# Kernel optimization log

Measured on AMD Instinct MI355X. Metric: run time of the kernel, lower is better.

The kernel has to match this reference:

```python
import jax, jax.numpy as jnp
import numpy as np
import math

E = 2048        # embed_dim
H = 16          # num_heads
HD = E // H // 2  # head_dim = 64
DEPTH = 12
LAMBDA_INIT = 0.8 - 0.6 * math.exp(-0.3 * DEPTH)


def setup_inputs() -> dict:
    key = jax.random.key(0)
    ks = jax.random.split(key, 9)
    s = 0.02
    return {
        "x": jax.random.normal(ks[0], (2, 2048, E), jnp.float32),
        "Wq": jax.random.normal(ks[1], (E, E), jnp.float32) * s,
        "Wk": jax.random.normal(ks[2], (E, E), jnp.float32) * s,  # n_rep = 1
        "Wv": jax.random.normal(ks[3], (E, E), jnp.float32) * s,
        "Wo": jax.random.normal(ks[4], (E, E), jnp.float32) * s,
        "lq1": jax.random.normal(ks[5], (HD,), jnp.float32) * 0.1,
        "lk1": jax.random.normal(ks[6], (HD,), jnp.float32) * 0.1,
        "lq2": jax.random.normal(ks[7], (HD,), jnp.float32) * 0.1,
        "lk2": jax.random.normal(ks[8], (HD,), jnp.float32) * 0.1,
    }


def reference(x, Wq, Wk, Wv, Wo, lq1, lk1, lq2, lk2):
    b, t, e = x.shape
    scaling = HD ** (-0.5)
    # projections; split into 2*H sub-heads of dim HD for q/k, H heads of 2*HD for v
    q = (x @ Wq).reshape(b, t, 2 * H, HD).transpose(0, 2, 1, 3) * scaling  # [b,2H,t,hd]
    k = (x @ Wk).reshape(b, t, 2 * H, HD).transpose(0, 2, 1, 3)           # [b,2H,t,hd]
    v = (x @ Wv).reshape(b, t, H, 2 * HD).transpose(0, 2, 1, 3)           # [b,H,t,2hd]

    scores = jnp.einsum('bhqd,bhkd->bhqk', q, k)  # [b,2H,t,t]
    causal = jnp.triu(jnp.full((t, t), -jnp.inf, dtype=jnp.float32), 1)
    aw = jax.nn.softmax((scores + causal).astype(jnp.float32), axis=-1)

    lam = (jnp.exp(jnp.sum(lq1 * lk1)) - jnp.exp(jnp.sum(lq2 * lk2)) + LAMBDA_INIT)
    aw = aw.reshape(b, H, 2, t, t)
    aw = aw[:, :, 0] - lam * aw[:, :, 1]  # differential attention

    attn = jnp.einsum('bhqk,bhkd->bhqd', aw, v)  # [b,H,t,2hd]
    # RMSNorm over last dim (no affine), eps=1e-5
    attn = attn * jax.lax.rsqrt(jnp.mean(attn * attn, axis=-1, keepdims=True) + 1e-5)
    attn = attn * (1.0 - LAMBDA_INIT)
    attn = attn.transpose(0, 2, 1, 3).reshape(b, t, H * 2 * HD)
    return attn @ Wo
```

## Files before the change

### kernel.cpp

```cpp
#include <hip/hip_runtime.h>
#include <stdint.h>

typedef __bf16 bf16_t;
typedef __bf16 bf16x8 __attribute__((ext_vector_type(8)));
typedef __bf16 bf16x4 __attribute__((ext_vector_type(4)));
typedef float  f32x4  __attribute__((ext_vector_type(4)));
typedef float  f32x16 __attribute__((ext_vector_type(16)));
typedef unsigned int u32;

#define L2E 1.44269504088896340736f
#define LAMBDA_INIT 0.7836057665316245f
#define ONE_MINUS_LAMBDA_INIT 0.2163942334683755f

__device__ __forceinline__ void gload_lds16(const void* g, void* l) {
  __builtin_amdgcn_global_load_lds(
      (const __attribute__((address_space(1))) char*)(uintptr_t)g,
      (__attribute__((address_space(3))) char*)(uintptr_t)l, 16, 0, 0);
}

__device__ __forceinline__ f32x4 mfma_bf16(bf16x8 a, bf16x8 b, f32x4 c) {
  return __builtin_amdgcn_mfma_f32_16x16x32_bf16(a, b, c, 0, 0, 0);
}
__device__ __forceinline__ f32x16 mfma32(bf16x8 a, bf16x8 b, f32x16 c) {
  return __builtin_amdgcn_mfma_f32_32x32x16_bf16(a, b, c, 0, 0, 0);
}

__device__ __forceinline__ u32 pkbf(float a, float b) {
  union { bf16_t h[2]; u32 u; } x;
  x.h[0] = (bf16_t)a; x.h[1] = (bf16_t)b;
  return x.u;
}
__device__ __forceinline__ void pl32swap(u32& a, u32& b) {
  asm volatile("v_permlane32_swap_b32 %0, %1" : "+v"(a), "+v"(b));
}

__global__ __launch_bounds__(256) void cvt_bf16(const float* __restrict__ in,
                                                bf16_t* __restrict__ out) {
  const size_t idx = ((size_t)blockIdx.x * 256 + threadIdx.x) * 8;
  float4 a = *(const float4*)(in + idx);
  float4 c = *(const float4*)(in + idx + 4);
  bf16x8 v;
  v[0] = (bf16_t)a.x; v[1] = (bf16_t)a.y; v[2] = (bf16_t)a.z; v[3] = (bf16_t)a.w;
  v[4] = (bf16_t)c.x; v[5] = (bf16_t)c.y; v[6] = (bf16_t)c.z; v[7] = (bf16_t)c.w;
  *(bf16x8*)(out + idx) = v;
}

struct WArgs {
  const float* W[4];
  bf16_t* WT[4];
  float sc[4];
};

__global__ __launch_bounds__(256) void cvt_wT_all(WArgs a) {
  __shared__ float t[64][65];
  const int i = blockIdx.z;
  const float* W = a.W[i];
  bf16_t* WT = a.WT[i];
  const float scale = a.sc[i];
  const int k0 = blockIdx.x * 64, n0 = blockIdx.y * 64;
  const int r = threadIdx.x >> 2, cg = threadIdx.x & 3;
#pragma unroll
  for (int q = 0; q < 4; ++q) {
    float4 v = *(const float4*)(W + (size_t)(k0 + r) * 2048 + n0 + cg * 16 + q * 4);
    t[r][cg * 16 + q * 4 + 0] = v.x;
    t[r][cg * 16 + q * 4 + 1] = v.y;
    t[r][cg * 16 + q * 4 + 2] = v.z;
    t[r][cg * 16 + q * 4 + 3] = v.w;
  }
  __syncthreads();
  bf16x8 o0, o1;
#pragma unroll
  for (int j = 0; j < 8; ++j) o0[j] = (bf16_t)(t[cg * 16 + j][r] * scale);
#pragma unroll
  for (int j = 0; j < 8; ++j) o1[j] = (bf16_t)(t[cg * 16 + 8 + j][r] * scale);
  bf16_t* dst = WT + (size_t)(n0 + r) * 2048 + k0 + cg * 16;
  *(bf16x8*)dst = o0;
  *(bf16x8*)(dst + 8) = o1;
}

__global__ void lam_kernel(const float* lq1, const float* lk1,
                           const float* lq2, const float* lk2, float* out) {
  const int l = threadIdx.x;
  float p1 = lq1[l] * lk1[l];
  float p2 = lq2[l] * lk2[l];
#pragma unroll
  for (int d = 1; d < 64; d <<= 1) {
    p1 += __shfl_xor(p1, d);
    p2 += __shfl_xor(p2, d);
  }
  if (l == 0) *out = expf(p1) - expf(p2) + LAMBDA_INIT;
}

__global__ __launch_bounds__(512, 2) void gemm256(const bf16_t* __restrict__ A,
                                                  const bf16_t* __restrict__ Bt,
                                                  bf16_t* __restrict__ Cqk) {
  extern __shared__ __align__(16) char sm[];
  const int tid = threadIdx.x;
  const int w = tid >> 6, lane = tid & 63;
  const int wr = w >> 2, wc = w & 3;
  const int lm = lane >> 4, ln = lane & 15;
  const int nwg = (int)(gridDim.x * gridDim.y);
  const int flat = (int)blockIdx.y * (int)gridDim.x + (int)blockIdx.x;
  const int swz = (flat & 7) * (nwg >> 3) + (flat >> 3);
  const int m0 = (swz & 15) * 256, n0 = (swz >> 4) * 256;

  int aoff[8], boff[4];
#pragma unroll
  for (int m = 0; m < 8; ++m) {
    const int row = wr * 128 + m * 16 + ln;
    aoff[m] = row * 64 + ((lm * 16) ^ ((((row >> 2) ^ row) & 3) << 4));
  }
#pragma unroll
  for (int n = 0; n < 4; ++n) {
    const int row = wc * 64 + n * 16 + ln;
    boff[n] = row * 64 + ((lm * 16) ^ ((((row >> 2) ^ row) & 3) << 4));
  }

  const bf16_t* gsrc[4];
  int ldst[4];
#pragma unroll
  for (int j = 0; j < 4; ++j) {
    const int r2 = j & 1, opB = j >> 1;
    const int row = r2 * 128 + w * 16 + (lane >> 2);
    const int colb = (lane & 3) * 16;
    const int cb = colb ^ ((((row >> 2) ^ row) & 3) << 4);
    gsrc[j] = (opB ? Bt + (size_t)(n0 + row) * 2048
                   : A + (size_t)(m0 + row) * 2048) + (cb >> 1);
    ldst[j] = opB * 16384 + r2 * 8192 + w * 1024;
  }

  const f32x4 vzero = {0.f, 0.f, 0.f, 0.f};
  f32x4 acc[8][4];
#pragma unroll
  for (int m = 0; m < 8; ++m)
#pragma unroll
    for (int n = 0; n < 4; ++n) acc[m][n] = vzero;

#pragma unroll
  for (int kt = 0; kt < 3; ++kt)
#pragma unroll
    for (int j = 0; j < 4; ++j)
      gload_lds16(gsrc[j] + kt * 32, sm + kt * 32768 + ldst[j]);
  asm volatile("s_waitcnt vmcnt(8)" ::: "memory");
  __builtin_amdgcn_s_barrier();

  for (int kt = 0; kt < 64; ++kt) {
    const char* sa = sm + (kt & 3) * 32768;
    const char* sb = sa + 16384;
    const int stage = kt + 3;
    char* sd = sm + (stage & 3) * 32768;
    bf16x8 bfr[4], af[4];

#pragma unroll
    for (int n = 0; n < 4; ++n) bfr[n] = *(const bf16x8*)(sb + boff[n]);
#pragma unroll
    for (int m = 0; m < 4; ++m) af[m] = *(const bf16x8*)(sa + aoff[m]);
    if (stage < 64) {
      gload_lds16(gsrc[0] + stage * 32, sd + ldst[0]);
      gload_lds16(gsrc[1] + stage * 32, sd + ldst[1]);
    }
    __builtin_amdgcn_s_barrier();
    __builtin_amdgcn_s_setprio(1);
#pragma unroll
    for (int m = 0; m < 4; ++m)
#pragma unroll
      for (int n = 0; n < 4; ++n) acc[m][n] = mfma_bf16(af[m], bfr[n], acc[m][n]);
    __builtin_amdgcn_s_setprio(0);
    __builtin_amdgcn_s_barrier();

#pragma unroll
    for (int m = 0; m < 4; ++m) af[m] = *(const bf16x8*)(sa + aoff[4 + m]);
    if (stage < 64) {
      gload_lds16(gsrc[2] + stage * 32, sd + ldst[2]);
      gload_lds16(gsrc[3] + stage * 32, sd + ldst[3]);
    }
    __builtin_amdgcn_s_barrier();
    __builtin_amdgcn_s_setprio(1);
#pragma unroll
    for (int m = 0; m < 4; ++m)
#pragma unroll
      for (int n = 0; n < 4; ++n)
        acc[4 + m][n] = mfma_bf16(af[m], bfr[n], acc[4 + m][n]);
    __builtin_amdgcn_s_setprio(0);
    if (kt < 61) {
      asm volatile("s_waitcnt vmcnt(8)" ::: "memory");
    } else if (kt == 61) {
      asm volatile("s_waitcnt vmcnt(4)" ::: "memory");
    } else if (kt == 62) {
      asm volatile("s_waitcnt vmcnt(0)" ::: "memory");
    }
    __builtin_amdgcn_s_barrier();
  }

  bf16_t* C = Cqk + (size_t)(n0 >> 11) * (4096u * 2048u);
#pragma unroll
  for (int m = 0; m < 8; ++m)
#pragma unroll
    for (int n = 0; n < 4; ++n)
#pragma unroll
      for (int r = 0; r < 4; ++r) {
        const size_t grow = m0 + wr * 128 + m * 16 + lm * 4 + r;
        const int gcol = (n0 + wc * 64 + n * 16 + ln) & 2047;
        C[grow * 2048 + gcol] = (bf16_t)acc[m][n][r];
      }
}

template <int OUTMODE>
__global__ __launch_bounds__(256, 2) void gemm_bt(const bf16_t* __restrict__ A,
                                                  const bf16_t* __restrict__ Bt,
                                                  void* __restrict__ Cv) {
  __shared__ __align__(16) bf16_t As[128 * 64];
  __shared__ __align__(16) bf16_t Bs[128 * 64];
  const int tid = threadIdx.x;
  const int w = tid >> 6, lane = tid & 63;
  const int wr = w >> 1, wc = w & 1;
  const int lm = lane >> 4, ln = lane & 15;
  const int nwg = (int)(gridDim.x * gridDim.y);
  const int flat = (int)blockIdx.y * (int)gridDim.x + (int)blockIdx.x;
  const int swz = (flat & 7) * (nwg >> 3) + (flat >> 3);
  const int m0 = (swz & 31) * 128, n0 = (swz >> 5) * 128;

  const f32x4 vzero = {0.f, 0.f, 0.f, 0.f};
  f32x4 acc[4][4];
#pragma unroll
  for (int m = 0; m < 4; ++m)
#pragma unroll
    for (int n = 0; n < 4; ++n) acc[m][n] = vzero;

  for (int k0 = 0; k0 < 2048; k0 += 64) {
    __syncthreads();
#pragma unroll
    for (int j = 0; j < 4; ++j) {
      const int inst = w * 4 + j;
      const int row = inst * 8 + (lane >> 3);
      const int cb = ((lane & 7) * 16) ^ ((row & 7) << 4);
      gload_lds16(A + (size_t)(m0 + row) * 2048 + k0 + (cb >> 1),
                  (char*)As + inst * 1024);
      gload_lds16(Bt + (size_t)(n0 + row) * 2048 + k0 + (cb >> 1),
                  (char*)Bs + inst * 1024);
    }
    asm volatile("s_waitcnt vmcnt(0)" ::: "memory");
    __syncthreads();

#pragma unroll
    for (int kc = 0; kc < 2; ++kc) {
      bf16x8 af[4], bfr[4];
#pragma unroll
      for (int m = 0; m < 4; ++m) {
        const int row = wr * 64 + m * 16 + ln;
        int off = row * 128 + kc * 64 + lm * 16;
        off ^= (row & 7) << 4;
        af[m] = *(const bf16x8*)((const char*)As + off);
      }
#pragma unroll
      for (int n = 0; n < 4; ++n) {
        const int row = wc * 64 + n * 16 + ln;
        int off = row * 128 + kc * 64 + lm * 16;
        off ^= (row & 7) << 4;
        bfr[n] = *(const bf16x8*)((const char*)Bs + off);
      }
      __builtin_amdgcn_s_setprio(1);
#pragma unroll
      for (int m = 0; m < 4; ++m)
#pragma unroll
        for (int n = 0; n < 4; ++n) acc[m][n] = mfma_bf16(af[m], bfr[n], acc[m][n]);
      __builtin_amdgcn_s_setprio(0);
    }
  }

  if (OUTMODE == 1) {
    bf16_t* C = (bf16_t*)Cv;
#pragma unroll
    for (int m = 0; m < 4; ++m) {
      const int growb = m0 + wr * 64 + m * 16 + lm * 4;
      const int bb = growb >> 11, t = growb & 2047;
      const int kt = t >> 6, kk = (t >> 4) & 3, hi2 = (t >> 3) & 1, e0 = t & 7;
#pragma unroll
      for (int n = 0; n < 4; ++n) {
        const int gcol = n0 + wc * 64 + n * 16 + ln;
        const int hh = gcol >> 7, g = (gcol >> 5) & 3, l31o = gcol & 31;
        bf16x4 v;
#pragma unroll
        for (int r = 0; r < 4; ++r) v[r] = (bf16_t)acc[m][n][r];
        const size_t idx = ((size_t)((bb * 16 + hh) * 32 + kt)) * 8192 +
                           (size_t)(((g * 4 + kk) * 64 + hi2 * 32 + l31o) * 8 + e0);
        *(bf16x4*)(C + idx) = v;
      }
    }
  } else {
    float* C = (float*)Cv;
#pragma unroll
    for (int m = 0; m < 4; ++m)
#pragma unroll
      for (int n = 0; n < 4; ++n)
#pragma unroll
        for (int r = 0; r < 4; ++r) {
          const size_t grow = m0 + wr * 64 + m * 16 + lm * 4 + r;
          const int gcol = n0 + wc * 64 + n * 16 + ln;
          C[grow * 2048 + gcol] = acc[m][n][r];
        }
  }
}

__global__ __launch_bounds__(256, 2) void flash_diff(const bf16_t* __restrict__ Q,
                                                     const bf16_t* __restrict__ K,
                                                     const bf16_t* __restrict__ Vf,
                                                     bf16_t* __restrict__ attnb,
                                                     const float* __restrict__ lamP) {
  __shared__ __align__(16) char smem[65536];

  const int tid = threadIdx.x;
  const int w = tid >> 6, lane = tid & 63;
  const int qh = w >> 1, s = w & 1;
  const int l31 = lane & 31, hi = lane >> 5;

  const int bid = (int)blockIdx.x;
  const int xcd = bid & 7, p = bid >> 3;
  const int qtp = p & 15, g2 = p >> 4;
  const int hb = g2 * 8 + xcd;
  const int h = hb & 15, b = hb >> 4;
  const size_t bt0 = (size_t)b * 2048;
  const float lam = *lamP;

  auto stage_k = [&](int buf, int k0) {
#pragma unroll
    for (int j = 0; j < 4; ++j) {
      const int inst = w * 4 + j;
      const int row = inst * 4 + (lane >> 4);
      const int cb = ((lane & 15) * 16) ^ ((row & 15) << 4);
      gload_lds16(K + (bt0 + k0 + row) * 2048 + h * 128 + (cb >> 1),
                  smem + buf * 16384 + inst * 1024);
    }
  };
  auto stage_v = [&](int buf, int kt) {
    const char* src = (const char*)Vf +
                      (((size_t)((b * 16 + h) * 32 + kt)) << 14) + lane * 16;
#pragma unroll
    for (int j = 0; j < 4; ++j) {
      const int inst = w * 4 + j;
      gload_lds16(src + inst * 1024, smem + 32768 + buf * 16384 + inst * 1024);
    }
  };

  for (int half = 0; half < 2; ++half) {
    const int qt = half == 0 ? qtp : 31 - qtp;
    const int q0 = qt * 64;
    const int qloc = qh * 32 + l31;

    bf16x8 qf[4];
#pragma unroll
    for (int kc = 0; kc < 4; ++kc)
      qf[kc] = *(const bf16x8*)(Q + (bt0 + q0 + qloc) * 2048 + h * 128 +
                                s * 64 + kc * 16 + hi * 8);

    stage_k(0, 0);
    stage_v(0, 0);
    asm volatile("s_waitcnt vmcnt(0)" ::: "memory");
    __syncthreads();

    f32x16 accv[4];
#pragma unroll
    for (int m = 0; m < 4; ++m)
#pragma unroll
      for (int r = 0; r < 16; ++r) accv[m][r] = 0.f;
    float lsum = 0.f;

    int cur = 0;
    for (int kt = 0; kt <= qt; ++kt) {
      if (kt < qt) {
        stage_k(cur ^ 1, (kt + 1) * 64);
        stage_v(cur ^ 1, kt + 1);
      }
      const char* Ksb = (const char*)smem + cur * 16384;
      const char* Vsb = (const char*)smem + 32768 + cur * 16384;

      bf16x8 pf[2][2];
#pragma unroll
      for (int mt = 0; mt < 2; ++mt) {
        f32x16 sa;
#pragma unroll
        for (int r = 0; r < 16; ++r) sa[r] = 0.f;
        const int row = mt * 32 + l31;
        const int rswz = (row & 15) << 4;
        __builtin_amdgcn_s_setprio(1);
#pragma unroll
        for (int kc = 0; kc < 4; ++kc) {
          int off = row * 256 + s * 128 + kc * 32 + hi * 16;
          off ^= rswz;
          bf16x8 kf = *(const bf16x8*)(Ksb + off);
          sa = mfma32(kf, qf[kc], sa);
        }
        __builtin_amdgcn_s_setprio(0);

        if (kt == qt) {
#pragma unroll
          for (int r = 0; r < 16; ++r) {
            const int key = mt * 32 + (r & 3) + 8 * (r >> 2) + 4 * hi;
            if (key > qloc) sa[r] = -1e30f;
          }
        }
        float pv[16];
#pragma unroll
        for (int r = 0; r < 16; ++r) {
          pv[r] = exp2f(sa[r]);
          lsum += pv[r];
        }
        u32 c0 = pkbf(pv[0], pv[1]),   c1 = pkbf(pv[2], pv[3]);
        u32 c2 = pkbf(pv[4], pv[5]),   c3 = pkbf(pv[6], pv[7]);
        u32 c4 = pkbf(pv[8], pv[9]),   c5 = pkbf(pv[10], pv[11]);
        u32 c6 = pkbf(pv[12], pv[13]), c7 = pkbf(pv[14], pv[15]);
        pl32swap(c0, c2); pl32swap(c1, c3);
        pl32swap(c4, c6); pl32swap(c5, c7);
        union { u32 u[4]; bf16x8 v; } f0, f1;
        f0.u[0] = c0; f0.u[1] = c1; f0.u[2] = c2; f0.u[3] = c3;
        f1.u[0] = c4; f1.u[1] = c5; f1.u[2] = c6; f1.u[3] = c7;
        pf[mt][0] = f0.v;
        pf[mt][1] = f1.v;
      }

#pragma unroll
      for (int g = 0; g < 4; ++g) {
        __builtin_amdgcn_s_setprio(1);
#pragma unroll
        for (int kk = 0; kk < 4; ++kk) {
          bf16x8 vfr = *(const bf16x8*)(Vsb + (g * 4 + kk) * 1024 + lane * 16);
          accv[g] = mfma32(vfr, pf[kk >> 1][kk & 1], accv[g]);
        }
        __builtin_amdgcn_s_setprio(0);
      }

      asm volatile("s_waitcnt vmcnt(0)" ::: "memory");
      __syncthreads();
      cur ^= 1;
    }

    lsum += __shfl_xor(lsum, 32);
    const float rl = 1.0f / lsum;
    float* Obuf = (float*)smem;

    if (s == 1) {
#pragma unroll
      for (int mt4 = 0; mt4 < 4; ++mt4)
#pragma unroll
        for (int q2 = 0; q2 < 4; ++q2) {
          f32x4 v;
#pragma unroll
          for (int e = 0; e < 4; ++e) v[e] = accv[mt4][q2 * 4 + e] * rl;
          const int d = mt4 * 32 + q2 * 8 + hi * 4;
          *(f32x4*)(Obuf + (size_t)qloc * 128 + d) = v;
        }
    }
    __syncthreads();
    if (s == 0) {
      float o[4][16];
      float ss = 0.f;
#pragma unroll
      for (int mt4 = 0; mt4 < 4; ++mt4)
#pragma unroll
        for (int q2 = 0; q2 < 4; ++q2) {
          const int d = mt4 * 32 + q2 * 8 + hi * 4;
          f32x4 ov = *(const f32x4*)(Obuf + (size_t)qloc * 128 + d);
#pragma unroll
          for (int e = 0; e < 4; ++e) {
            const float v = accv[mt4][q2 * 4 + e] * rl - lam * ov[e];
            o[mt4][q2 * 4 + e] = v;
            ss += v * v;
          }
        }
      ss += __shfl_xor(ss, 32);
      const float sc = rsqrtf(ss * (1.0f / 128.f) + 1e-5f) * ONE_MINUS_LAMBDA_INIT;
      const size_t grow = bt0 + q0 + qloc;
#pragma unroll
      for (int mt4 = 0; mt4 < 4; ++mt4)
#pragma unroll
        for (int q2 = 0; q2 < 4; ++q2) {
          const int d = mt4 * 32 + q2 * 8 + hi * 4;
          bf16x4 v;
#pragma unroll
          for (int e = 0; e < 4; ++e) v[e] = (bf16_t)(o[mt4][q2 * 4 + e] * sc);
          *(bf16x4*)(attnb + grow * 2048 + h * 128 + d) = v;
        }
    }
    __syncthreads();
  }
}

extern "C" void kernel_launch(void* const* d_in, const int* in_sizes, int n_in,
                              void* d_out, int out_size, void* d_ws, size_t ws_size,
                              hipStream_t stream) {
  const float* x   = (const float*)d_in[0];
  const float* Wq  = (const float*)d_in[1];
  const float* Wk  = (const float*)d_in[2];
  const float* Wv  = (const float*)d_in[3];
  const float* Wo  = (const float*)d_in[4];
  const float* lq1 = (const float*)d_in[5];
  const float* lk1 = (const float*)d_in[6];
  const float* lq2 = (const float*)d_in[7];
  const float* lk2 = (const float*)d_in[8];

  char* ws = (char*)d_ws;
  bf16_t* xb    = (bf16_t*)(ws + 0);
  bf16_t* wqT   = (bf16_t*)(ws + 16777216);
  bf16_t* wvT   = (bf16_t*)(ws + 33554432);
  bf16_t* woT   = (bf16_t*)(ws + 41943040);
  bf16_t* Qb    = (bf16_t*)(ws + 50331648);
  bf16_t* Kb    = (bf16_t*)(ws + 67108864);
  bf16_t* Vfb   = (bf16_t*)(ws + 16777216);
  bf16_t* attnb = (bf16_t*)(ws + 0);
  float*  lamP  = (float*)(ws + 83886080);

  hipFuncSetAttribute((const void*)gemm256,
                      hipFuncAttributeMaxDynamicSharedMemorySize, 131072);

  cvt_bf16<<<4096, 256, 0, stream>>>(x, xb);
  WArgs wa;
  wa.W[0] = Wq; wa.W[1] = Wk; wa.W[2] = Wv; wa.W[3] = Wo;
  wa.WT[0] = wqT; wa.WT[1] = wqT + 4194304; wa.WT[2] = wvT; wa.WT[3] = woT;
  wa.sc[0] = 0.125f * L2E; wa.sc[1] = 1.0f; wa.sc[2] = 1.0f; wa.sc[3] = 1.0f;
  cvt_wT_all<<<dim3(32, 32, 4), 256, 0, stream>>>(wa);
  lam_kernel<<<1, 64, 0, stream>>>(lq1, lk1, lq2, lk2, lamP);

  gemm256<<<dim3(16, 16), 512, 131072, stream>>>(xb, wqT, Qb);
  gemm_bt<1><<<dim3(32, 16), 256, 0, stream>>>(xb, wvT, (void*)Vfb);

  flash_diff<<<512, 256, 0, stream>>>(Qb, Kb, Vfb, attnb, lamP);

  gemm_bt<2><<<dim3(32, 16), 256, 0, stream>>>(attnb, woT, d_out);
}
```

Before: 263.3 us.

## Replace 128x128 GEMM with 256x128 tile, 4-stage async LDS pipeline

The V and output projection GEMMs move from a 128x128 tile with synchronous single-buffered loads to a 256x128 tile run by 8 waves. A 4-stage ring buffer in dynamic LDS, with a K step of 32, issues global-to-LDS loads three steps ahead and interleaves them with the MFMA halves. The goal is to hide global memory latency and raise operand reuse per block. In exchange it uses 96KB of LDS per block and more barriers per iteration. Whether two blocks can fit per CU is not established.

```diff
diff --git a/kernel.cpp b/kernel.cpp
--- a/kernel.cpp
+++ b/kernel.cpp
@@ -206,11 +206,10 @@
 }
 
 template <int OUTMODE>
-__global__ __launch_bounds__(256, 2) void gemm_bt(const bf16_t* __restrict__ A,
-                                                  const bf16_t* __restrict__ Bt,
-                                                  void* __restrict__ Cv) {
-  __shared__ __align__(16) bf16_t As[128 * 64];
-  __shared__ __align__(16) bf16_t Bs[128 * 64];
+__global__ __launch_bounds__(512, 2) void gemm256n(const bf16_t* __restrict__ A,
+                                                   const bf16_t* __restrict__ Bt,
+                                                   void* __restrict__ Cv) {
+  extern __shared__ __align__(16) char sm[];
   const int tid = threadIdx.x;
   const int w = tid >> 6, lane = tid & 63;
   const int wr = w >> 1, wc = w & 1;
@@ -218,7 +217,32 @@
   const int nwg = (int)(gridDim.x * gridDim.y);
   const int flat = (int)blockIdx.y * (int)gridDim.x + (int)blockIdx.x;
   const int swz = (flat & 7) * (nwg >> 3) + (flat >> 3);
-  const int m0 = (swz & 31) * 128, n0 = (swz >> 5) * 128;
+  const int m0 = (swz & 15) * 256, n0 = (swz >> 4) * 128;
+
+  int aoff[4], boff[4];
+#pragma unroll
+  for (int m = 0; m < 4; ++m) {
+    const int row = wr * 64 + m * 16 + ln;
+    aoff[m] = row * 64 + ((lm * 16) ^ ((((row >> 2) ^ row) & 3) << 4));
+  }
+#pragma unroll
+  for (int n = 0; n < 4; ++n) {
+    const int row = wc * 64 + n * 16 + ln;
+    boff[n] = row * 64 + ((lm * 16) ^ ((((row >> 2) ^ row) & 3) << 4));
+  }
+
+  const bf16_t* gsrc[3];
+  int ldst[3];
+#pragma unroll
+  for (int j = 0; j < 3; ++j) {
+    const int r2 = j & 1, opB = j >> 1;
+    const int row = (opB ? 0 : r2 * 128) + w * 16 + (lane >> 2);
+    const int colb = (lane & 3) * 16;
+    const int cb = colb ^ ((((row >> 2) ^ row) & 3) << 4);
+    gsrc[j] = (opB ? Bt + (size_t)(n0 + row) * 2048
+                   : A + (size_t)(m0 + row) * 2048) + (cb >> 1);
+    ldst[j] = opB * 16384 + (opB ? 0 : r2 * 8192) + w * 1024;
+  }
 
   const f32x4 vzero = {0.f, 0.f, 0.f, 0.f};
   f32x4 acc[4][4];
@@ -227,45 +251,58 @@
 #pragma unroll
     for (int n = 0; n < 4; ++n) acc[m][n] = vzero;
 
-  for (int k0 = 0; k0 < 2048; k0 += 64) {
-    __syncthreads();
-#pragma unroll
-    for (int j = 0; j < 4; ++j) {
-      const int inst = w * 4 + j;
-      const int row = inst * 8 + (lane >> 3);
-      const int cb = ((lane & 7) * 16) ^ ((row & 7) << 4);
-      gload_lds16(A + (size_t)(m0 + row) * 2048 + k0 + (cb >> 1),
-                  (char*)As + inst * 1024);
-      gload_lds16(Bt + (size_t)(n0 + row) * 2048 + k0 + (cb >> 1),
-                  (char*)Bs + inst * 1024);
-    }
-    asm volatile("s_waitcnt vmcnt(0)" ::: "memory");
-    __syncthreads();
-
-#pragma unroll
-    for (int kc = 0; kc < 2; ++kc) {
-      bf16x8 af[4], bfr[4];
-#pragma unroll
-      for (int m = 0; m < 4; ++m) {
-        const int row = wr * 64 + m * 16 + ln;
-        int off = row * 128 + kc * 64 + lm * 16;
-        off ^= (row & 7) << 4;
-        af[m] = *(const bf16x8*)((const char*)As + off);
-      }
-#pragma unroll
-      for (int n = 0; n < 4; ++n) {
-        const int row = wc * 64 + n * 16 + ln;
-        int off = row * 128 + kc * 64 + lm * 16;
-        off ^= (row & 7) << 4;
-        bfr[n] = *(const bf16x8*)((const char*)Bs + off);
-      }
-      __builtin_amdgcn_s_setprio(1);
-#pragma unroll
-      for (int m = 0; m < 4; ++m)
-#pragma unroll
-        for (int n = 0; n < 4; ++n) acc[m][n] = mfma_bf16(af[m], bfr[n], acc[m][n]);
-      __builtin_amdgcn_s_setprio(0);
-    }
+#pragma unroll
+  for (int kt = 0; kt < 3; ++kt)
+#pragma unroll
+    for (int j = 0; j < 3; ++j)
+      gload_lds16(gsrc[j] + kt * 32, sm + kt * 24576 + ldst[j]);
+  asm volatile("s_waitcnt vmcnt(6)" ::: "memory");
+  __builtin_amdgcn_s_barrier();
+
+  for (int kt = 0; kt < 64; ++kt) {
+    const char* sa = sm + (kt & 3) * 24576;
+    const char* sb = sa + 16384;
+    const int stage = kt + 3;
+    char* sd = sm + (stage & 3) * 24576;
+    bf16x8 bfr[4], af[4];
+
+#pragma unroll
+    for (int n = 0; n < 4; ++n) bfr[n] = *(const bf16x8*)(sb + boff[n]);
+    af[0] = *(const bf16x8*)(sa + aoff[0]);
+    af[1] = *(const bf16x8*)(sa + aoff[1]);
+    if (stage < 64) {
+      gload_lds16(gsrc[0] + stage * 32, sd + ldst[0]);
+      gload_lds16(gsrc[1] + stage * 32, sd + ldst[1]);
+    }
+    __builtin_amdgcn_s_barrier();
+    __builtin_amdgcn_s_setprio(1);
+#pragma unroll
+    for (int m = 0; m < 2; ++m)
+#pragma unroll
+      for (int n = 0; n < 4; ++n) acc[m][n] = mfma_bf16(af[m], bfr[n], acc[m][n]);
+    __builtin_amdgcn_s_setprio(0);
+    __builtin_amdgcn_s_barrier();
+
+    af[2] = *(const bf16x8*)(sa + aoff[2]);
+    af[3] = *(const bf16x8*)(sa + aoff[3]);
+    if (stage < 64) {
+      gload_lds16(gsrc[2] + stage * 32, sd + ldst[2]);
+    }
+    __builtin_amdgcn_s_barrier();
+    __builtin_amdgcn_s_setprio(1);
+#pragma unroll
+    for (int m = 2; m < 4; ++m)
+#pragma unroll
+      for (int n = 0; n < 4; ++n) acc[m][n] = mfma_bf16(af[m], bfr[n], acc[m][n]);
+    __builtin_amdgcn_s_setprio(0);
+    if (kt < 61) {
+      asm volatile("s_waitcnt vmcnt(6)" ::: "memory");
+    } else if (kt == 61) {
+      asm volatile("s_waitcnt vmcnt(3)" ::: "memory");
+    } else if (kt == 62) {
+      asm volatile("s_waitcnt vmcnt(0)" ::: "memory");
+    }
+    __builtin_amdgcn_s_barrier();
   }
 
   if (OUTMODE == 1) {
@@ -511,6 +548,10 @@
 
   hipFuncSetAttribute((const void*)gemm256,
                       hipFuncAttributeMaxDynamicSharedMemorySize, 131072);
+  hipFuncSetAttribute((const void*)gemm256n<1>,
+                      hipFuncAttributeMaxDynamicSharedMemorySize, 98304);
+  hipFuncSetAttribute((const void*)gemm256n<2>,
+                      hipFuncAttributeMaxDynamicSharedMemorySize, 98304);
 
   cvt_bf16<<<4096, 256, 0, stream>>>(x, xb);
   WArgs wa;
@@ -521,9 +562,9 @@
   lam_kernel<<<1, 64, 0, stream>>>(lq1, lk1, lq2, lk2, lamP);
 
   gemm256<<<dim3(16, 16), 512, 131072, stream>>>(xb, wqT, Qb);
-  gemm_bt<1><<<dim3(32, 16), 256, 0, stream>>>(xb, wvT, (void*)Vfb);
+  gemm256n<1><<<dim3(16, 16), 512, 98304, stream>>>(xb, wvT, (void*)Vfb);
 
   flash_diff<<<512, 256, 0, stream>>>(Qb, Kb, Vfb, attnb, lamP);
 
-  gemm_bt<2><<<dim3(32, 16), 256, 0, stream>>>(attnb, woT, d_out);
-}
+  gemm256n<2><<<dim3(16, 16), 512, 98304, stream>>>(attnb, woT, d_out);
+}
```

Measured after the change: 269.9 us. +2.5%, slower.
